# Optimization experiments

Measured on AMD Instinct MI355X. Metric: run time of the kernel, lower is better.

The kernel has to match this reference:

```python
import jax, jax.numpy as jnp
import numpy as np

DIM, HEADS, MLP_RATIO = 384, 6, 4.0
HEAD_DIM = DIM // HEADS
HID = int(DIM * MLP_RATIO)
EPS = 1e-5


def _layer_norm(x, g, b):
    m = jnp.mean(x, axis=-1, keepdims=True)
    v = jnp.mean(jnp.square(x - m), axis=-1, keepdims=True)
    return (x - m) * jax.lax.rsqrt(v + EPS) * g + b


def setup_inputs() -> dict:
    key = jax.random.key(0)
    ks = jax.random.split(key, 16)
    B, N, C = 4, 2048, DIM
    s = 0.02
    return {
        "x": jax.random.normal(ks[0], (B, N, C), dtype=jnp.float32),
        "ln1_g": jnp.ones((C,), jnp.float32),
        "ln1_b": jnp.zeros((C,), jnp.float32),
        "qkv_w": jax.random.normal(ks[1], (C, 3 * C), jnp.float32) * s,  # [in, out]
        "qkv_b": jnp.zeros((3 * C,), jnp.float32),
        "proj_w": jax.random.normal(ks[2], (C, C), jnp.float32) * s,
        "proj_b": jnp.zeros((C,), jnp.float32),
        "ln2_g": jnp.ones((C,), jnp.float32),
        "ln2_b": jnp.zeros((C,), jnp.float32),
        "fc1_w": jax.random.normal(ks[3], (C, HID), jnp.float32) * s,
        "fc1_b": jnp.zeros((HID,), jnp.float32),
        "fc2_w": jax.random.normal(ks[4], (HID, C), jnp.float32) * s,
        "fc2_b": jnp.zeros((C,), jnp.float32),
    }


def reference(x, ln1_g, ln1_b, qkv_w, qkv_b, proj_w, proj_b,
              ln2_g, ln2_b, fc1_w, fc1_b, fc2_w, fc2_b):
    B, N, C = x.shape
    scale = HEAD_DIM ** (-0.5)

    # --- attention branch (pre-norm) ---
    h = _layer_norm(x, ln1_g, ln1_b)
    qkv = (h @ qkv_w + qkv_b).reshape(B, N, 3, HEADS, HEAD_DIM)
    qkv = jnp.transpose(qkv, (2, 0, 3, 1, 4))  # [3, B, H, N, D]
    q, k, v = qkv[0], qkv[1], qkv[2]
    attn = jnp.einsum("bhnd,bhmd->bhnm", q, k) * scale
    attn = jax.nn.softmax(attn, axis=-1)
    out = jnp.einsum("bhnm,bhmd->bhnd", attn, v)
    out = jnp.transpose(out, (0, 2, 1, 3)).reshape(B, N, C)
    x = x + (out @ proj_w + proj_b)

    # --- MLP branch (pre-norm) ---
    h = _layer_norm(x, ln2_g, ln2_b)
    h = jax.nn.gelu(h @ fc1_w + fc1_b, approximate=False)
    x = x + (h @ fc2_w + fc2_b)
    return x
```

## Files before the change

kernel.cpp:

```cpp
#include <hip/hip_runtime.h>

typedef unsigned short u16;
typedef unsigned int u32;
typedef __bf16 bf16x8_t __attribute__((ext_vector_type(8)));
typedef float f32x4 __attribute__((ext_vector_type(4)));
typedef float f32x16 __attribute__((ext_vector_type(16)));

__device__ __forceinline__ u16 f2b(float f) {
  union { float f; u32 u; } v; v.f = f;
  u32 r = v.u + 0x7fffu + ((v.u >> 16) & 1u);
  return (u16)(r >> 16);
}

__device__ __forceinline__ u32 pkbf(float a, float b) {
  union { __bf16 h[2]; u32 u; } v;
  v.h[0] = (__bf16)a; v.h[1] = (__bf16)b;
  return v.u;
}

__device__ __forceinline__ size_t fmoff(int r, int c, int Kd) {
  return ((size_t)(r >> 4) * (Kd >> 3) + (c >> 3)) * 128 + (r & 15) * 8 + (c & 7);
}

__device__ __forceinline__ f32x4 mfma16(uint4 a, uint4 b, f32x4 c) {
  return __builtin_amdgcn_mfma_f32_16x16x32_bf16(
      __builtin_bit_cast(bf16x8_t, a), __builtin_bit_cast(bf16x8_t, b), c, 0, 0, 0);
}

__device__ __forceinline__ f32x16 mfma32(uint4 a, uint4 b, f32x16 c) {
  return __builtin_amdgcn_mfma_f32_32x32x16_bf16(
      __builtin_bit_cast(bf16x8_t, a), __builtin_bit_cast(bf16x8_t, b), c, 0, 0, 0);
}

__device__ __forceinline__ void plswap(u32& a, u32& b) {
  asm("v_permlane32_swap_b32 %0, %1" : "+v"(a), "+v"(b));
}

__device__ __forceinline__ void load_lds16(const void* g, void* l) {
  __builtin_amdgcn_global_load_lds(
      (const __attribute__((address_space(1))) unsigned int*)g,
      (__attribute__((address_space(3))) unsigned int*)l, 16, 0, 0);
}

template <int N>
__device__ __forceinline__ void waitvm() {
  if constexpr (N == 0) asm volatile("s_waitcnt vmcnt(0)" ::: "memory");
  else if constexpr (N == 4) asm volatile("s_waitcnt vmcnt(4)" ::: "memory");
  else if constexpr (N == 6) asm volatile("s_waitcnt vmcnt(6)" ::: "memory");
  else if constexpr (N == 8) asm volatile("s_waitcnt vmcnt(8)" ::: "memory");
  else asm volatile("s_waitcnt vmcnt(10)" ::: "memory");
}

__device__ __forceinline__ void ln_body(const float* __restrict__ x,
                                        const float* __restrict__ g,
                                        const float* __restrict__ bta,
                                        u16* __restrict__ out, int row,
                                        int lane) {
  const float* xr = x + (size_t)row * 384;
  float v[6];
  float s = 0.f;
#pragma unroll
  for (int i = 0; i < 6; i++) { v[i] = xr[i * 64 + lane]; s += v[i]; }
#pragma unroll
  for (int off = 32; off >= 1; off >>= 1) s += __shfl_xor(s, off);
  float mean = s * (1.0f / 384.0f);
  float vs = 0.f;
#pragma unroll
  for (int i = 0; i < 6; i++) { float d = v[i] - mean; vs += d * d; }
#pragma unroll
  for (int off = 32; off >= 1; off >>= 1) vs += __shfl_xor(vs, off);
  float rstd = rsqrtf(vs * (1.0f / 384.0f) + 1e-5f);
#pragma unroll
  for (int i = 0; i < 6; i++) {
    int c = i * 64 + lane;
    out[fmoff(row, c, 384)] = f2b((v[i] - mean) * rstd * g[c] + bta[c]);
  }
}

__global__ __launch_bounds__(256) void ln_k(const float* __restrict__ x,
                                            const float* __restrict__ g,
                                            const float* __restrict__ bta,
                                            u16* __restrict__ out) {
  ln_body(x, g, bta, out, blockIdx.x * 4 + (threadIdx.x >> 6),
          threadIdx.x & 63);
}

__global__ __launch_bounds__(256) void prep_k(
    const float* __restrict__ w0, u16* __restrict__ t0_,
    const float* __restrict__ w1, u16* __restrict__ t1_,
    const float* __restrict__ w2, u16* __restrict__ t2_,
    const float* __restrict__ w3, u16* __restrict__ t3_,
    const float* __restrict__ x, const float* __restrict__ g,
    const float* __restrict__ bta, u16* __restrict__ lnout) {
  __shared__ u16 L[64][68];
  int tile = blockIdx.x, tid = threadIdx.x;
  if (tile >= 432) {
    ln_body(x, g, bta, lnout, (tile - 432) * 4 + (tid >> 6), tid & 63);
    return;
  }
  const float* w; u16* wt; int K, N, rel;
  if (tile < 108)      { w = w0; wt = t0_; K = 384;  N = 1152; rel = tile; }
  else if (tile < 144) { w = w1; wt = t1_; K = 384;  N = 384;  rel = tile - 108; }
  else if (tile < 288) { w = w2; wt = t2_; K = 384;  N = 1536; rel = tile - 144; }
  else                 { w = w3; wt = t3_; K = 1536; N = 384;  rel = tile - 288; }
  int ntx = N >> 6;
  int tk = (rel / ntx) << 6, tn = (rel - (rel / ntx) * ntx) << 6;

  int r = tid >> 2, c0 = (tid & 3) << 4;
  const float* src = w + (size_t)(tk + r) * N + tn + c0;
#pragma unroll
  for (int j = 0; j < 16; j += 4) {
    float4 a = *(const float4*)(src + j);
    L[r][c0 + j + 0] = f2b(a.x);
    L[r][c0 + j + 1] = f2b(a.y);
    L[r][c0 + j + 2] = f2b(a.z);
    L[r][c0 + j + 3] = f2b(a.w);
  }
  __syncthreads();
  int n = tid >> 2, k0 = (tid & 3) << 4;
  u16 tmp[16];
#pragma unroll
  for (int j = 0; j < 16; j++) tmp[j] = L[k0 + j][n];
  u16* dst = wt + (size_t)(tn + n) * K + tk + k0;
  *(uint4*)dst = *(const uint4*)(tmp);
  *(uint4*)(dst + 8) = *(const uint4*)(tmp + 8);
}

template <int EPI, int MR, int KD, int NX, int MINW>
__global__ __launch_bounds__(256, MINW) void gemm_k(
    const u16* __restrict__ A, const u16* __restrict__ Bt,
    const float* __restrict__ bias, const float* __restrict__ res,
    void* __restrict__ outp, int Nn,
    u16* __restrict__ qp, u16* __restrict__ kp, u16* __restrict__ vtp) {
  constexpr int NS = KD / 64;
  constexpr int KD8 = KD / 8;
  __shared__ __align__(16) u16 Bs[3][64 * 64];
  int tid = threadIdx.x;
  int lane = tid & 63, wid = tid >> 6;
  int li = lane & 15, lg = lane >> 4;
  int wr = wid >> 1, wc = wid & 1;

  int p = blockIdx.x;
  int idx = p >> 3;
  int cx = idx % NX;
  int row0 = ((p & 7) + ((idx / NX) << 3)) * (MR * 32);
  int col0 = cx * 64;

  int lr = lane >> 3;
  int sc8 = ((lane & 7) ^ lr) * 8;

  const u16* Ab = A + ((size_t)(row0 / 16 + wr * MR) * KD8 + lg) * 128 + li * 8;

  f32x4 z = {0.f, 0.f, 0.f, 0.f};
  f32x4 acc[MR][2];
#pragma unroll
  for (int m = 0; m < MR; m++)
#pragma unroll
    for (int n = 0; n < 2; n++) acc[m][n] = z;

  uint4 af0[MR][2], af1[MR][2];

  auto stageB = [&](int buf, int k0) {
#pragma unroll
    for (int j = 0; j < 2; j++) {
      int ib = wid * 2 + j;
      load_lds16(Bt + (size_t)(col0 + ib * 8 + lr) * KD + k0 + sc8,
                 (char*)Bs[buf] + ib * 1024);
    }
  };
  auto loadA = [&](uint4 (*dst)[2], int t) {
#pragma unroll
    for (int m = 0; m < MR; m++)
#pragma unroll
      for (int kk = 0; kk < 2; kk++)
        dst[m][kk] =
            *(const uint4*)(Ab + ((size_t)m * KD8 + t * 8 + kk * 4) * 128);
  };

  stageB(0, 0);
  stageB(1, 64);
  loadA(af0, 0);
  if (NS > 1) loadA(af1, 1);
  waitvm<2 * MR>();
  __builtin_amdgcn_s_barrier();
  asm volatile("" ::: "memory");

#pragma unroll
  for (int t = 0; t < NS; t++) {
    if (t + 2 < NS) stageB((t + 2) % 3, (t + 2) * 64);
    const char* Bsb = (const char*)Bs[t % 3];
#pragma unroll
    for (int kk = 0; kk < 2; kk++) {
      uint4 bf[2];
#pragma unroll
      for (int n = 0; n < 2; n++) {
        int c = wc * 32 + n * 16 + li;
        bf[n] = *(const uint4*)(Bsb + c * 128 +
                                ((kk * 64 + lg * 16) ^ ((c & 7) << 4)));
      }
#pragma unroll
      for (int m = 0; m < MR; m++)
#pragma unroll
        for (int n = 0; n < 2; n++)
          acc[m][n] = mfma16((t & 1) ? af1[m][kk] : af0[m][kk], bf[n],
                             acc[m][n]);
    }
    if (t + 2 < NS) {
      if (t & 1) loadA(af1, t + 2);
      else       loadA(af0, t + 2);
      waitvm<2 + 2 * MR>();
      __builtin_amdgcn_s_barrier();
      asm volatile("" ::: "memory");
    } else if (t + 1 < NS) {
      waitvm<0>();
      __builtin_amdgcn_s_barrier();
      asm volatile("" ::: "memory");
    }
  }

#pragma unroll
  for (int m = 0; m < MR; m++) {
#pragma unroll
    for (int n = 0; n < 2; n++) {
#pragma unroll
      for (int j = 0; j < 4; j++) {
        int r = row0 + wr * (MR * 16) + m * 16 + lg * 4 + j;
        int c = col0 + wc * 32 + n * 16 + li;
        float v = acc[m][n][j] + bias[c];
        if (EPI == 0) {
          ((float*)outp)[(size_t)r * Nn + c] = v + res[(size_t)r * Nn + c];
        } else if (EPI == 1) {
          float e = __expf(-1.5957691f * v * (1.f + 0.044715f * v * v));
          ((u16*)outp)[fmoff(r, c, Nn)] = f2b(v / (1.f + e));
        } else {
          int tt = c / 384;
          int c2 = c - tt * 384;
          int hh = c2 >> 6, d = c2 & 63;
          int bb = r >> 11, nn = r & 2047;
          size_t bh = (size_t)bb * 6 + hh;
          int tile = nn >> 5;
          if (tt == 2) {
            int kvl = nn & 31;
            int kvHalf = (kvl >> 4) & 1, h2 = (kvl >> 3) & 1, jj = kvl & 7;
            int dTile = d >> 5, l31 = d & 31;
            vtp[(((bh * 64 + tile) * 2 + dTile) * 2 + kvHalf) * 512 +
                (l31 + h2 * 32) * 8 + jj] = f2b(v);
          } else {
            int chunk = d >> 4, h2 = (d >> 3) & 1, e = d & 7;
            int l31 = nn & 31;
            size_t off = ((bh * 64 + tile) * 4 + chunk) * 512 +
                         (l31 + h2 * 32) * 8 + e;
            if (tt == 0) qp[off] = f2b(v * 0.18033688f);
            else         kp[off] = f2b(v);
          }
        }
      }
    }
  }
}

__global__ __launch_bounds__(256, 2) void attn_k(const u16* __restrict__ q,
                                                 const u16* __restrict__ k,
                                                 const u16* __restrict__ vt,
                                                 u16* __restrict__ out) {
  __shared__ __align__(16) float Ol[3][2][16][64];
  __shared__ float Ls[3][64];

  int tid = threadIdx.x;
  int lane = tid & 63, wid = tid >> 6;
  int l31 = lane & 31, hi = lane >> 5;
  int bid = blockIdx.x;
  int nid = (bid & 7) * 96 + (bid >> 3);
  int bh = nid >> 5, qT = nid & 31;
  int b = bh / 6, hh = bh - b * 6;
  int qb = qT * 64;

  const u16* qp_ = q + ((size_t)bh * 64 + qT * 2) * 2048 + lane * 8;
  const u16* kp_ = k + ((size_t)bh * 64 + wid * 16) * 2048 + lane * 8;
  const u16* vp_ = vt + ((size_t)bh * 64 + wid * 16) * 2048 + lane * 8;

  uint4 qf0[4], qf1[4], kf[4];
#pragma unroll
  for (int c = 0; c < 4; c++) qf0[c] = *(const uint4*)(qp_ + c * 512);
#pragma unroll
  for (int c = 0; c < 4; c++) qf1[c] = *(const uint4*)(qp_ + 2048 + c * 512);
#pragma unroll
  for (int c = 0; c < 4; c++) kf[c] = *(const uint4*)(kp_ + c * 512);
  kp_ += 2048;

  f32x16 o00, o01, o10, o11;
#pragma unroll
  for (int r = 0; r < 16; r++) {
    o00[r] = 0.f; o01[r] = 0.f; o10[r] = 0.f; o11[r] = 0.f;
  }
  float ls0 = 0.f, ls1 = 0.f;

#pragma unroll
  for (int t = 0; t < 16; t++) {
    uint4 vf0 = *(const uint4*)(vp_);
    uint4 vf1 = *(const uint4*)(vp_ + 512);
    uint4 vf2 = *(const uint4*)(vp_ + 1024);
    uint4 vf3 = *(const uint4*)(vp_ + 1536);
    uint4 kn[4];
    if (t < 15) {
#pragma unroll
      for (int c = 0; c < 4; c++) kn[c] = *(const uint4*)(kp_ + c * 512);
    }

    {
      f32x16 s;
#pragma unroll
      for (int r = 0; r < 16; r++) s[r] = 0.f;
#pragma unroll
      for (int c = 0; c < 4; c++) s = mfma32(kf[c], qf0[c], s);
      float p[16];
#pragma unroll
      for (int r = 0; r < 16; r++) p[r] = __builtin_amdgcn_exp2f(s[r]);
      ls0 += ((p[0] + p[1]) + (p[2] + p[3])) + ((p[4] + p[5]) + (p[6] + p[7])) +
             ((p[8] + p[9]) + (p[10] + p[11])) +
             ((p[12] + p[13]) + (p[14] + p[15]));
      u32 u[8];
#pragma unroll
      for (int i = 0; i < 8; i++) u[i] = pkbf(p[2 * i], p[2 * i + 1]);
      plswap(u[0], u[2]); plswap(u[1], u[3]);
      plswap(u[4], u[6]); plswap(u[5], u[7]);
      uint4 pa0 = {u[0], u[1], u[2], u[3]};
      uint4 pa1 = {u[4], u[5], u[6], u[7]};
      o00 = mfma32(pa0, vf0, o00);
      o00 = mfma32(pa1, vf1, o00);
      o01 = mfma32(pa0, vf2, o01);
      o01 = mfma32(pa1, vf3, o01);
    }
    {
      f32x16 s;
#pragma unroll
      for (int r = 0; r < 16; r++) s[r] = 0.f;
#pragma unroll
      for (int c = 0; c < 4; c++) s = mfma32(kf[c], qf1[c], s);
      float p[16];
#pragma unroll
      for (int r = 0; r < 16; r++) p[r] = __builtin_amdgcn_exp2f(s[r]);
      ls1 += ((p[0] + p[1]) + (p[2] + p[3])) + ((p[4] + p[5]) + (p[6] + p[7])) +
             ((p[8] + p[9]) + (p[10] + p[11])) +
             ((p[12] + p[13]) + (p[14] + p[15]));
      u32 u[8];
#pragma unroll
      for (int i = 0; i < 8; i++) u[i] = pkbf(p[2 * i], p[2 * i + 1]);
      plswap(u[0], u[2]); plswap(u[1], u[3]);
      plswap(u[4], u[6]); plswap(u[5], u[7]);
      uint4 pa0 = {u[0], u[1], u[2], u[3]};
      uint4 pa1 = {u[4], u[5], u[6], u[7]};
      o10 = mfma32(pa0, vf0, o10);
      o10 = mfma32(pa1, vf1, o10);
      o11 = mfma32(pa0, vf2, o11);
      o11 = mfma32(pa1, vf3, o11);
    }

    if (t < 15) {
#pragma unroll
      for (int c = 0; c < 4; c++) kf[c] = kn[c];
    }
    kp_ += 2048;
    vp_ += 2048;
  }

  ls0 += __shfl_xor(ls0, 32);
  ls1 += __shfl_xor(ls1, 32);

  if (wid) {
#pragma unroll
    for (int r = 0; r < 16; r++) {
      Ol[wid - 1][0][r][lane] = o00[r];
      Ol[wid - 1][1][r][lane] = o01[r];
    }
    Ls[wid - 1][lane] = ls0;
  }
  __syncthreads();
  if (wid == 0) {
#pragma unroll
    for (int w = 0; w < 3; w++) ls0 += Ls[w][lane];
#pragma unroll
    for (int r = 0; r < 16; r++)
#pragma unroll
      for (int w = 0; w < 3; w++) {
        o00[r] += Ol[w][0][r][lane];
        o01[r] += Ol[w][1][r][lane];
      }
    float rl = 1.0f / ls0;
#pragma unroll
    for (int r = 0; r < 16; r++) {
      int qo = (r & 3) + 8 * (r >> 2) + hi * 4;
      float rlq = __shfl(rl, qo, 64);
      int row = b * 2048 + qb + qo;
      out[fmoff(row, hh * 64 + l31, 384)] = f2b(o00[r] * rlq);
      out[fmoff(row, hh * 64 + 32 + l31, 384)] = f2b(o01[r] * rlq);
    }
  }
  __syncthreads();
  if (wid) {
#pragma unroll
    for (int r = 0; r < 16; r++) {
      Ol[wid - 1][0][r][lane] = o10[r];
      Ol[wid - 1][1][r][lane] = o11[r];
    }
    Ls[wid - 1][lane] = ls1;
  }
  __syncthreads();
  if (wid == 0) {
#pragma unroll
    for (int w = 0; w < 3; w++) ls1 += Ls[w][lane];
#pragma unroll
    for (int r = 0; r < 16; r++)
#pragma unroll
      for (int w = 0; w < 3; w++) {
        o10[r] += Ol[w][0][r][lane];
        o11[r] += Ol[w][1][r][lane];
      }
    float rl = 1.0f / ls1;
#pragma unroll
    for (int r = 0; r < 16; r++) {
      int qo = (r & 3) + 8 * (r >> 2) + hi * 4;
      float rlq = __shfl(rl, qo, 64);
      int row = b * 2048 + qb + 32 + qo;
      out[fmoff(row, hh * 64 + l31, 384)] = f2b(o10[r] * rlq);
      out[fmoff(row, hh * 64 + 32 + l31, 384)] = f2b(o11[r] * rlq);
    }
  }
}

extern "C" void kernel_launch(void* const* d_in, const int* in_sizes, int n_in,
                              void* d_out, int out_size, void* d_ws,
                              size_t ws_size, hipStream_t stream) {
  const float* x      = (const float*)d_in[0];
  const float* ln1_g  = (const float*)d_in[1];
  const float* ln1_b  = (const float*)d_in[2];
  const float* qkv_w  = (const float*)d_in[3];
  const float* qkv_b  = (const float*)d_in[4];
  const float* proj_w = (const float*)d_in[5];
  const float* proj_b = (const float*)d_in[6];
  const float* ln2_g  = (const float*)d_in[7];
  const float* ln2_b  = (const float*)d_in[8];
  const float* fc1_w  = (const float*)d_in[9];
  const float* fc1_b  = (const float*)d_in[10];
  const float* fc2_w  = (const float*)d_in[11];
  const float* fc2_b  = (const float*)d_in[12];
  float* out = (float*)d_out;

  char* p = (char*)d_ws;
  u16* qkvwt  = (u16*)p;  p += (size_t)1152 * 384 * 2;
  u16* projwt = (u16*)p;  p += (size_t)384 * 384 * 2;
  u16* fc1wt  = (u16*)p;  p += (size_t)1536 * 384 * 2;
  u16* fc2wt  = (u16*)p;  p += (size_t)384 * 1536 * 2;
  float* x1   = (float*)p; p += (size_t)8192 * 384 * 4;
  u16* reg1   = (u16*)p;  p += (size_t)8192 * 384 * 2;
  u16* reg2   = (u16*)p;  p += (size_t)8192 * 1536 * 2;
  u16* qd  = reg2;
  u16* kd  = reg2 + (size_t)24 * 2048 * 64;
  u16* vtd = kd + (size_t)24 * 2048 * 64;
  u16* h3  = reg2;

  prep_k<<<432 + 2048, 256, 0, stream>>>(qkv_w, qkvwt, proj_w, projwt,
                                         fc1_w, fc1wt, fc2_w, fc2wt,
                                         x, ln1_g, ln1_b, reg1);
  gemm_k<2, 4, 384, 18, 2><<<dim3(1152), 256, 0, stream>>>(
      reg1, qkvwt, qkv_b, nullptr, nullptr, 1152, qd, kd, vtd);
  attn_k<<<dim3(768), 256, 0, stream>>>(qd, kd, vtd, reg1);
  gemm_k<0, 2, 384, 6, 4><<<dim3(768), 256, 0, stream>>>(
      reg1, projwt, proj_b, x, x1, 384, nullptr, nullptr, nullptr);
  ln_k<<<2048, 256, 0, stream>>>(x1, ln2_g, ln2_b, reg1);
  gemm_k<1, 4, 384, 24, 2><<<dim3(1536), 256, 0, stream>>>(
      reg1, fc1wt, fc1_b, nullptr, h3, 1536, nullptr, nullptr, nullptr);
  gemm_k<0, 2, 1536, 6, 4><<<dim3(768), 256, 0, stream>>>(
      h3, fc2wt, fc2_b, x1, out, 384, nullptr, nullptr, nullptr);
}
```

Measured before the change: 120.6 us.

## Load GEMM B operands directly into registers from fragment-major layout; prefetch V

The weight-transpose kernel now writes the transposed bf16 weights in the same 16x8 fragment-major layout used for A. The GEMM therefore loads B fragments straight from global memory into registers with double buffering, in place of the triple-buffered LDS staging with barriers and vmcnt waits. The attention kernel also software-prefetches the next V tile alongside the next K tile. This removes LDS traffic and barrier synchronisation, at the cost of redundant global/L2 reads of B across waves and more register pressure.

```diff
diff --git a/kernel.cpp b/kernel.cpp
--- a/kernel.cpp
+++ b/kernel.cpp
@@ -34,21 +34,6 @@
 
 __device__ __forceinline__ void plswap(u32& a, u32& b) {
   asm("v_permlane32_swap_b32 %0, %1" : "+v"(a), "+v"(b));
-}
-
-__device__ __forceinline__ void load_lds16(const void* g, void* l) {
-  __builtin_amdgcn_global_load_lds(
-      (const __attribute__((address_space(1))) unsigned int*)g,
-      (__attribute__((address_space(3))) unsigned int*)l, 16, 0, 0);
-}
-
-template <int N>
-__device__ __forceinline__ void waitvm() {
-  if constexpr (N == 0) asm volatile("s_waitcnt vmcnt(0)" ::: "memory");
-  else if constexpr (N == 4) asm volatile("s_waitcnt vmcnt(4)" ::: "memory");
-  else if constexpr (N == 6) asm volatile("s_waitcnt vmcnt(6)" ::: "memory");
-  else if constexpr (N == 8) asm volatile("s_waitcnt vmcnt(8)" ::: "memory");
-  else asm volatile("s_waitcnt vmcnt(10)" ::: "memory");
 }
 
 __device__ __forceinline__ void ln_body(const float* __restrict__ x,
@@ -121,9 +106,9 @@
   u16 tmp[16];
 #pragma unroll
   for (int j = 0; j < 16; j++) tmp[j] = L[k0 + j][n];
-  u16* dst = wt + (size_t)(tn + n) * K + tk + k0;
+  u16* dst = wt + fmoff(tn + n, tk + k0, K);
   *(uint4*)dst = *(const uint4*)(tmp);
-  *(uint4*)(dst + 8) = *(const uint4*)(tmp + 8);
+  *(uint4*)(dst + 128) = *(const uint4*)(tmp + 8);
 }
 
 template <int EPI, int MR, int KD, int NX, int MINW>
@@ -134,7 +119,6 @@
     u16* __restrict__ qp, u16* __restrict__ kp, u16* __restrict__ vtp) {
   constexpr int NS = KD / 64;
   constexpr int KD8 = KD / 8;
-  __shared__ __align__(16) u16 Bs[3][64 * 64];
   int tid = threadIdx.x;
   int lane = tid & 63, wid = tid >> 6;
   int li = lane & 15, lg = lane >> 4;
@@ -146,10 +130,8 @@
   int row0 = ((p & 7) + ((idx / NX) << 3)) * (MR * 32);
   int col0 = cx * 64;
 
-  int lr = lane >> 3;
-  int sc8 = ((lane & 7) ^ lr) * 8;
-
   const u16* Ab = A + ((size_t)(row0 / 16 + wr * MR) * KD8 + lg) * 128 + li * 8;
+  const u16* Bb = Bt + ((size_t)(col0 / 16 + wc * 2) * KD8 + lg) * 128 + li * 8;
 
   f32x4 z = {0.f, 0.f, 0.f, 0.f};
   f32x4 acc[MR][2];
@@ -158,16 +140,8 @@
 #pragma unroll
     for (int n = 0; n < 2; n++) acc[m][n] = z;
 
-  uint4 af0[MR][2], af1[MR][2];
-
-  auto stageB = [&](int buf, int k0) {
-#pragma unroll
-    for (int j = 0; j < 2; j++) {
-      int ib = wid * 2 + j;
-      load_lds16(Bt + (size_t)(col0 + ib * 8 + lr) * KD + k0 + sc8,
-                 (char*)Bs[buf] + ib * 1024);
-    }
-  };
+  uint4 af0[MR][2], af1[MR][2], bf0[2][2], bf1[2][2];
+
   auto loadA = [&](uint4 (*dst)[2], int t) {
 #pragma unroll
     for (int m = 0; m < MR; m++)
@@ -176,46 +150,32 @@
         dst[m][kk] =
             *(const uint4*)(Ab + ((size_t)m * KD8 + t * 8 + kk * 4) * 128);
   };
-
-  stageB(0, 0);
-  stageB(1, 64);
+  auto loadB = [&](uint4 (*dst)[2], int t) {
+#pragma unroll
+    for (int n = 0; n < 2; n++)
+#pragma unroll
+      for (int kk = 0; kk < 2; kk++)
+        dst[n][kk] =
+            *(const uint4*)(Bb + ((size_t)n * KD8 + t * 8 + kk * 4) * 128);
+  };
+
   loadA(af0, 0);
-  if (NS > 1) loadA(af1, 1);
-  waitvm<2 * MR>();
-  __builtin_amdgcn_s_barrier();
-  asm volatile("" ::: "memory");
+  loadB(bf0, 0);
 
 #pragma unroll
   for (int t = 0; t < NS; t++) {
-    if (t + 2 < NS) stageB((t + 2) % 3, (t + 2) * 64);
-    const char* Bsb = (const char*)Bs[t % 3];
-#pragma unroll
-    for (int kk = 0; kk < 2; kk++) {
-      uint4 bf[2];
-#pragma unroll
-      for (int n = 0; n < 2; n++) {
-        int c = wc * 32 + n * 16 + li;
-        bf[n] = *(const uint4*)(Bsb + c * 128 +
-                                ((kk * 64 + lg * 16) ^ ((c & 7) << 4)));
-      }
+    if (t + 1 < NS) {
+      if (t & 1) { loadA(af0, t + 1); loadB(bf0, t + 1); }
+      else       { loadA(af1, t + 1); loadB(bf1, t + 1); }
+    }
+#pragma unroll
+    for (int kk = 0; kk < 2; kk++)
 #pragma unroll
       for (int m = 0; m < MR; m++)
 #pragma unroll
         for (int n = 0; n < 2; n++)
-          acc[m][n] = mfma16((t & 1) ? af1[m][kk] : af0[m][kk], bf[n],
-                             acc[m][n]);
-    }
-    if (t + 2 < NS) {
-      if (t & 1) loadA(af1, t + 2);
-      else       loadA(af0, t + 2);
-      waitvm<2 + 2 * MR>();
-      __builtin_amdgcn_s_barrier();
-      asm volatile("" ::: "memory");
-    } else if (t + 1 < NS) {
-      waitvm<0>();
-      __builtin_amdgcn_s_barrier();
-      asm volatile("" ::: "memory");
-    }
+          acc[m][n] = mfma16((t & 1) ? af1[m][kk] : af0[m][kk],
+                             (t & 1) ? bf1[n][kk] : bf0[n][kk], acc[m][n]);
   }
 
 #pragma unroll
@@ -279,14 +239,17 @@
   const u16* kp_ = k + ((size_t)bh * 64 + wid * 16) * 2048 + lane * 8;
   const u16* vp_ = vt + ((size_t)bh * 64 + wid * 16) * 2048 + lane * 8;
 
-  uint4 qf0[4], qf1[4], kf[4];
+  uint4 qf0[4], qf1[4], kf[4], vf[4];
 #pragma unroll
   for (int c = 0; c < 4; c++) qf0[c] = *(const uint4*)(qp_ + c * 512);
 #pragma unroll
   for (int c = 0; c < 4; c++) qf1[c] = *(const uint4*)(qp_ + 2048 + c * 512);
 #pragma unroll
   for (int c = 0; c < 4; c++) kf[c] = *(const uint4*)(kp_ + c * 512);
+#pragma unroll
+  for (int c = 0; c < 4; c++) vf[c] = *(const uint4*)(vp_ + c * 512);
   kp_ += 2048;
+  vp_ += 2048;
 
   f32x16 o00, o01, o10, o11;
 #pragma unroll
@@ -297,14 +260,12 @@
 
 #pragma unroll
   for (int t = 0; t < 16; t++) {
-    uint4 vf0 = *(const uint4*)(vp_);
-    uint4 vf1 = *(const uint4*)(vp_ + 512);
-    uint4 vf2 = *(const uint4*)(vp_ + 1024);
-    uint4 vf3 = *(const uint4*)(vp_ + 1536);
-    uint4 kn[4];
+    uint4 kn[4], vn[4];
     if (t < 15) {
 #pragma unroll
       for (int c = 0; c < 4; c++) kn[c] = *(const uint4*)(kp_ + c * 512);
+#pragma unroll
+      for (int c = 0; c < 4; c++) vn[c] = *(const uint4*)(vp_ + c * 512);
     }
 
     {
@@ -326,10 +287,10 @@
       plswap(u[4], u[6]); plswap(u[5], u[7]);
       uint4 pa0 = {u[0], u[1], u[2], u[3]};
       uint4 pa1 = {u[4], u[5], u[6], u[7]};
-      o00 = mfma32(pa0, vf0, o00);
-      o00 = mfma32(pa1, vf1, o00);
-      o01 = mfma32(pa0, vf2, o01);
-      o01 = mfma32(pa1, vf3, o01);
+      o00 = mfma32(pa0, vf[0], o00);
+      o00 = mfma32(pa1, vf[1], o00);
+      o01 = mfma32(pa0, vf[2], o01);
+      o01 = mfma32(pa1, vf[3], o01);
     }
     {
       f32x16 s;
@@ -350,15 +311,15 @@
       plswap(u[4], u[6]); plswap(u[5], u[7]);
       uint4 pa0 = {u[0], u[1], u[2], u[3]};
       uint4 pa1 = {u[4], u[5], u[6], u[7]};
-      o10 = mfma32(pa0, vf0, o10);
-      o10 = mfma32(pa1, vf1, o10);
-      o11 = mfma32(pa0, vf2, o11);
-      o11 = mfma32(pa1, vf3, o11);
+      o10 = mfma32(pa0, vf[0], o10);
+      o10 = mfma32(pa1, vf[1], o10);
+      o11 = mfma32(pa0, vf[2], o11);
+      o11 = mfma32(pa1, vf[3], o11);
     }
 
     if (t < 15) {
 #pragma unroll
-      for (int c = 0; c < 4; c++) kf[c] = kn[c];
+      for (int c = 0; c < 4; c++) { kf[c] = kn[c]; vf[c] = vn[c]; }
     }
     kp_ += 2048;
     vp_ += 2048;
```

Result: slower. 127.0 us (+5.3%).

## Pre-tile proj/fc2 weights in fragment layout and use LDS-free thin GEMM

Applied to the files above, without the earlier changes.

The weight prep kernel now writes the proj and fc2 transposed weights in the MFMA fragment-major layout. A new thin GEMM kernel loads both A and B fragments straight from global memory into registers with double buffering. This drops the shared-memory staging and barriers for the two N=384 residual GEMMs. The cost is more redundant global/L2 traffic per block and more register pressure, since B fragments are re-read by every row block without LDS sharing.

```diff
diff --git a/kernel.cpp b/kernel.cpp
--- a/kernel.cpp
+++ b/kernel.cpp
@@ -98,11 +98,11 @@
     ln_body(x, g, bta, lnout, (tile - 432) * 4 + (tid >> 6), tid & 63);
     return;
   }
-  const float* w; u16* wt; int K, N, rel;
-  if (tile < 108)      { w = w0; wt = t0_; K = 384;  N = 1152; rel = tile; }
-  else if (tile < 144) { w = w1; wt = t1_; K = 384;  N = 384;  rel = tile - 108; }
-  else if (tile < 288) { w = w2; wt = t2_; K = 384;  N = 1536; rel = tile - 144; }
-  else                 { w = w3; wt = t3_; K = 1536; N = 384;  rel = tile - 288; }
+  const float* w; u16* wt; int K, N, rel; bool fm;
+  if (tile < 108)      { w = w0; wt = t0_; K = 384;  N = 1152; rel = tile;       fm = false; }
+  else if (tile < 144) { w = w1; wt = t1_; K = 384;  N = 384;  rel = tile - 108; fm = true; }
+  else if (tile < 288) { w = w2; wt = t2_; K = 384;  N = 1536; rel = tile - 144; fm = false; }
+  else                 { w = w3; wt = t3_; K = 1536; N = 384;  rel = tile - 288; fm = true; }
   int ntx = N >> 6;
   int tk = (rel / ntx) << 6, tn = (rel - (rel / ntx) * ntx) << 6;
 
@@ -121,9 +121,15 @@
   u16 tmp[16];
 #pragma unroll
   for (int j = 0; j < 16; j++) tmp[j] = L[k0 + j][n];
-  u16* dst = wt + (size_t)(tn + n) * K + tk + k0;
-  *(uint4*)dst = *(const uint4*)(tmp);
-  *(uint4*)(dst + 8) = *(const uint4*)(tmp + 8);
+  if (fm) {
+    u16* dst = wt + fmoff(tn + n, tk + k0, K);
+    *(uint4*)dst = *(const uint4*)(tmp);
+    *(uint4*)(dst + 128) = *(const uint4*)(tmp + 8);
+  } else {
+    u16* dst = wt + (size_t)(tn + n) * K + tk + k0;
+    *(uint4*)dst = *(const uint4*)(tmp);
+    *(uint4*)(dst + 8) = *(const uint4*)(tmp + 8);
+  }
 }
 
 template <int EPI, int MR, int KD, int NX, int MINW>
@@ -227,9 +233,7 @@
         int r = row0 + wr * (MR * 16) + m * 16 + lg * 4 + j;
         int c = col0 + wc * 32 + n * 16 + li;
         float v = acc[m][n][j] + bias[c];
-        if (EPI == 0) {
-          ((float*)outp)[(size_t)r * Nn + c] = v + res[(size_t)r * Nn + c];
-        } else if (EPI == 1) {
+        if (EPI == 1) {
           float e = __expf(-1.5957691f * v * (1.f + 0.044715f * v * v));
           ((u16*)outp)[fmoff(r, c, Nn)] = f2b(v / (1.f + e));
         } else {
@@ -259,6 +263,85 @@
   }
 }
 
+template <int KD, int NX, int MINW>
+__global__ __launch_bounds__(256, MINW) void gemm_thin_k(
+    const u16* __restrict__ A, const u16* __restrict__ Bt,
+    const float* __restrict__ bias, const float* __restrict__ res,
+    float* __restrict__ outp, int Nn) {
+  constexpr int NS = KD / 64;
+  constexpr int KD8 = KD / 8;
+  int tid = threadIdx.x;
+  int lane = tid & 63, wid = tid >> 6;
+  int li = lane & 15, lg = lane >> 4;
+  int wr = wid >> 1, wc = wid & 1;
+
+  int p = blockIdx.x;
+  int idx = p >> 3;
+  int cx = idx % NX;
+  int row0 = ((p & 7) + ((idx / NX) << 3)) * 64;
+  int col0 = cx * 64;
+
+  const u16* Ab = A + ((size_t)(row0 / 16 + wr * 2) * KD8 + lg) * 128 + li * 8;
+  const u16* Bb = Bt + ((size_t)(col0 / 16 + wc * 2) * KD8 + lg) * 128 + li * 8;
+
+  f32x4 z = {0.f, 0.f, 0.f, 0.f};
+  f32x4 acc[2][2];
+#pragma unroll
+  for (int m = 0; m < 2; m++)
+#pragma unroll
+    for (int n = 0; n < 2; n++) acc[m][n] = z;
+
+  uint4 af0[2][2], af1[2][2], bf0[2][2], bf1[2][2];
+
+  auto loadA = [&](uint4 (*dst)[2], int t) {
+#pragma unroll
+    for (int m = 0; m < 2; m++)
+#pragma unroll
+      for (int kk = 0; kk < 2; kk++)
+        dst[m][kk] =
+            *(const uint4*)(Ab + ((size_t)m * KD8 + t * 8 + kk * 4) * 128);
+  };
+  auto loadB = [&](uint4 (*dst)[2], int t) {
+#pragma unroll
+    for (int n = 0; n < 2; n++)
+#pragma unroll
+      for (int kk = 0; kk < 2; kk++)
+        dst[n][kk] =
+            *(const uint4*)(Bb + ((size_t)n * KD8 + t * 8 + kk * 4) * 128);
+  };
+
+  loadA(af0, 0);
+  loadB(bf0, 0);
+
+#pragma unroll
+  for (int t = 0; t < NS; t++) {
+    if (t + 1 < NS) {
+      if (t & 1) { loadA(af0, t + 1); loadB(bf0, t + 1); }
+      else       { loadA(af1, t + 1); loadB(bf1, t + 1); }
+    }
+#pragma unroll
+    for (int kk = 0; kk < 2; kk++)
+#pragma unroll
+      for (int m = 0; m < 2; m++)
+#pragma unroll
+        for (int n = 0; n < 2; n++)
+          acc[m][n] = mfma16((t & 1) ? af1[m][kk] : af0[m][kk],
+                             (t & 1) ? bf1[n][kk] : bf0[n][kk], acc[m][n]);
+  }
+
+#pragma unroll
+  for (int m = 0; m < 2; m++)
+#pragma unroll
+    for (int n = 0; n < 2; n++)
+#pragma unroll
+      for (int j = 0; j < 4; j++) {
+        int r = row0 + wr * 32 + m * 16 + lg * 4 + j;
+        int c = col0 + wc * 32 + n * 16 + li;
+        float v = acc[m][n][j] + bias[c];
+        outp[(size_t)r * Nn + c] = v + res[(size_t)r * Nn + c];
+      }
+}
+
 __global__ __launch_bounds__(256, 2) void attn_k(const u16* __restrict__ q,
                                                  const u16* __restrict__ k,
                                                  const u16* __restrict__ vt,
@@ -465,11 +548,11 @@
   gemm_k<2, 4, 384, 18, 2><<<dim3(1152), 256, 0, stream>>>(
       reg1, qkvwt, qkv_b, nullptr, nullptr, 1152, qd, kd, vtd);
   attn_k<<<dim3(768), 256, 0, stream>>>(qd, kd, vtd, reg1);
-  gemm_k<0, 2, 384, 6, 4><<<dim3(768), 256, 0, stream>>>(
-      reg1, projwt, proj_b, x, x1, 384, nullptr, nullptr, nullptr);
+  gemm_thin_k<384, 6, 4><<<dim3(768), 256, 0, stream>>>(
+      reg1, projwt, proj_b, x, x1, 384);
   ln_k<<<2048, 256, 0, stream>>>(x1, ln2_g, ln2_b, reg1);
   gemm_k<1, 4, 384, 24, 2><<<dim3(1536), 256, 0, stream>>>(
       reg1, fc1wt, fc1_b, nullptr, h3, 1536, nullptr, nullptr, nullptr);
-  gemm_k<0, 2, 1536, 6, 4><<<dim3(768), 256, 0, stream>>>(
-      h3, fc2wt, fc2_b, x1, out, 384, nullptr, nullptr, nullptr);
-}
+  gemm_thin_k<1536, 6, 4><<<dim3(768), 256, 0, stream>>>(
+      h3, fc2wt, fc2_b, x1, out, 384);
+}
```

Result: slower. 124.6 us (+3.4%).
